# Kernel tuning notes

Measured on AMD Instinct MI355X. Metric: run time of the kernel, lower is better.

Reference implementation:

```python
import jax, jax.numpy as jnp
import numpy as np

EPS = 1e-6
OHEM_RATIO = 3
NUM_KERNELS = 6
ALPHA = 0.5


def _dice_loss(inp, tgt, mask):
    # inp/tgt/mask: [B, H, W] -> scalar mean over batch
    B = inp.shape[0]
    i = (inp * mask).reshape(B, -1)
    t = (tgt * mask).reshape(B, -1)
    inter = jnp.sum(i * t, axis=1)
    union = jnp.sum(i * i, axis=1) + jnp.sum(t * t, axis=1) + EPS
    return jnp.mean(1.0 - 2.0 * inter / union)


def _ohem_mask(pred_prob, gt, tmask, ratio=OHEM_RATIO):
    # Vectorized per-sample OHEM: keep all positives plus the top
    # min(ratio*n_pos, n_neg) highest-scoring negatives.
    B, H, W = pred_prob.shape
    p = pred_prob.reshape(B, -1)
    g = gt.reshape(B, -1)
    m = tmask.reshape(B, -1)
    pos = (g > 0.5) & (m > 0.5)
    neg = (g <= 0.5) & (m > 0.5)
    n_pos = jnp.sum(pos, axis=1)
    n_neg = jnp.minimum(ratio * n_pos, jnp.sum(neg, axis=1))  # [B]
    scores = jnp.where(neg, p, -jnp.inf)
    # descending rank of each pixel's score within its sample
    order = jnp.argsort(-scores, axis=1)
    rank = jnp.argsort(order, axis=1)
    hard_neg = neg & (rank < n_neg[:, None])
    return (pos | hard_neg).astype(jnp.float32).reshape(B, H, W)


def setup_inputs() -> dict:
    key = jax.random.key(0)
    k1, k2, k3, k4 = jax.random.split(key, 4)
    B, C, H, W = 16, 6, 640, 640
    pred = jax.random.normal(k1, (B, C, H, W), dtype=jnp.float32)
    gt_text = (jax.random.uniform(k2, (B, 1, H, W)) > 0.9).astype(jnp.float32)
    gt_kernels = (jax.random.uniform(k3, (B, C - 1, H, W)) > 0.9).astype(jnp.float32)
    training_mask = (jax.random.uniform(k4, (B, 1, H, W)) > 0.05).astype(jnp.float32)
    return {"pred": pred, "gt_text": gt_text, "gt_kernels": gt_kernels,
            "training_mask": training_mask}


def reference(pred, gt_text, gt_kernels, training_mask):
    pred_text = pred[:, 0, :, :]                 # [B,H,W]
    pred_kernels = pred[:, 1:, :, :]             # [B,K,H,W]
    gt_text = gt_text[:, 0, :, :]                # squeeze(1)
    tmask = training_mask[:, 0, :, :]

    # original computes sigmoid + OHEM under no_grad -> stop_gradient
    pred_prob = jax.lax.stop_gradient(jax.nn.sigmoid(pred_text))
    ohem = jax.lax.stop_gradient(_ohem_mask(pred_prob, gt_text, tmask))

    loss_text = _dice_loss(pred_prob, gt_text, ohem)

    # vectorized dice over the K=num_kernels-1 kernel maps, mask broadcast
    pk = jax.nn.sigmoid(pred_kernels)            # [B,K,H,W]
    m = tmask[:, None, :, :]
    i = pk * m
    t = gt_kernels * m
    inter = jnp.sum(i * t, axis=(2, 3))          # [B,K]
    union = jnp.sum(i * i, axis=(2, 3)) + jnp.sum(t * t, axis=(2, 3)) + EPS
    # mean over kernels of (mean over batch) == mean over (B,K)
    loss_kernels = jnp.mean(1.0 - 2.0 * inter / union)

    loss = loss_kernels + ALPHA * loss_text
    return (loss, loss_text, loss_kernels)
```

## Files before the change

kernel.cpp:

```cpp
#include <hip/hip_runtime.h>
#include <math.h>

#define HW 409600
#define BB 16
#define CPRED 6
#define NKER 5
#define NBINS 2048
#define CHUNKS 128
#define EPSF 1e-6f

__device__ __forceinline__ float sigmoidf_(float x) {
    return 1.0f / (1.0f + __expf(-x));
}

__device__ __forceinline__ void proc_text(float m, float x, float g,
    float& n_pos, float& n_neg, float& sp, float& sp2,
    float* s_cnt, float* s_p2)
{
    if (m > 0.5f) {
        float p = sigmoidf_(x);
        if (g > 0.5f) {
            n_pos += 1.f; sp += p; sp2 += p * p;
        } else {
            n_neg += 1.f;
            int bin = (int)(p * (float)NBINS);
            bin = bin < 0 ? 0 : (bin > NBINS - 1 ? NBINS - 1 : bin);
            atomicAdd(&s_cnt[bin], 1.f);
            atomicAdd(&s_p2[bin], p * p);
        }
    }
}

__global__ __launch_bounds__(256) void pass1_kernel(
    const float* __restrict__ pred, const float* __restrict__ gt_text,
    const float* __restrict__ gt_k, const float* __restrict__ tmask,
    float* __restrict__ hist_cnt, float* __restrict__ hist_p2,
    float* __restrict__ bstats, float* __restrict__ kstats)
{
    __shared__ float s_cnt[NBINS];
    __shared__ float s_p2[NBINS];
    __shared__ float s_red[19][4];

    const int b = blockIdx.y;
    const int chunk = blockIdx.x;
    const int tid = threadIdx.x;

    for (int i = tid; i < NBINS; i += 256) { s_cnt[i] = 0.f; s_p2[i] = 0.f; }
    __syncthreads();

    const int NV4 = HW / 4;
    const float4* tm4 = reinterpret_cast<const float4*>(tmask + (size_t)b * HW);
    const float4* gt4 = reinterpret_cast<const float4*>(gt_text + (size_t)b * HW);
    const float4* pt4 = reinterpret_cast<const float4*>(pred + (size_t)b * CPRED * HW);
    const float4* gk4 = reinterpret_cast<const float4*>(gt_k + (size_t)b * NKER * HW);

    const int per = NV4 / CHUNKS;
    const int i0 = chunk * per;
    const int i1 = i0 + per;

    float n_pos = 0.f, n_neg = 0.f, sp = 0.f, sp2 = 0.f;
    float kin[NKER], kui[NKER], kut[NKER];
    #pragma unroll
    for (int c = 0; c < NKER; ++c) { kin[c] = 0.f; kui[c] = 0.f; kut[c] = 0.f; }

    for (int i = i0 + tid; i < i1; i += 256) {
        float4 m4 = tm4[i];
        float4 g4 = gt4[i];
        float4 x4 = pt4[i];

        proc_text(m4.x, x4.x, g4.x, n_pos, n_neg, sp, sp2, s_cnt, s_p2);
        proc_text(m4.y, x4.y, g4.y, n_pos, n_neg, sp, sp2, s_cnt, s_p2);
        proc_text(m4.z, x4.z, g4.z, n_pos, n_neg, sp, sp2, s_cnt, s_p2);
        proc_text(m4.w, x4.w, g4.w, n_pos, n_neg, sp, sp2, s_cnt, s_p2);

        float mb0 = m4.x > 0.5f ? 1.f : 0.f;
        float mb1 = m4.y > 0.5f ? 1.f : 0.f;
        float mb2 = m4.z > 0.5f ? 1.f : 0.f;
        float mb3 = m4.w > 0.5f ? 1.f : 0.f;

        #pragma unroll
        for (int c = 0; c < NKER; ++c) {
            float4 xk = pt4[(size_t)(c + 1) * NV4 + i];
            float4 gg = gk4[(size_t)c * NV4 + i];
            float p0 = sigmoidf_(xk.x), p1 = sigmoidf_(xk.y);
            float p2 = sigmoidf_(xk.z), p3 = sigmoidf_(xk.w);
            kin[c] += mb0 * p0 * gg.x + mb1 * p1 * gg.y
                    + mb2 * p2 * gg.z + mb3 * p3 * gg.w;
            kui[c] += mb0 * p0 * p0 + mb1 * p1 * p1
                    + mb2 * p2 * p2 + mb3 * p3 * p3;
            kut[c] += mb0 * gg.x + mb1 * gg.y + mb2 * gg.z + mb3 * gg.w;
        }
    }

    const int lane = tid & 63;
    const int wv = tid >> 6;
    #define WRED(v) { for (int o_ = 32; o_ > 0; o_ >>= 1) v += __shfl_down(v, o_, 64); }
    WRED(n_pos) WRED(n_neg) WRED(sp) WRED(sp2)
    if (lane == 0) {
        s_red[0][wv] = n_pos; s_red[1][wv] = n_neg;
        s_red[2][wv] = sp;    s_red[3][wv] = sp2;
    }
    #pragma unroll
    for (int c = 0; c < NKER; ++c) {
        float a = kin[c], u = kui[c], t = kut[c];
        WRED(a) WRED(u) WRED(t)
        if (lane == 0) {
            s_red[4 + c * 3 + 0][wv] = a;
            s_red[4 + c * 3 + 1][wv] = u;
            s_red[4 + c * 3 + 2][wv] = t;
        }
    }
    #undef WRED
    __syncthreads();

    if (tid < 19) {
        float a = s_red[tid][0] + s_red[tid][1] + s_red[tid][2] + s_red[tid][3];
        float* dst;
        if (tid < 4) dst = &bstats[b * 4 + tid];
        else {
            int q = tid - 4;
            dst = &kstats[(b * NKER + q / 3) * 3 + (q % 3)];
        }
        atomicAdd(dst, a);
    }

    for (int i = tid; i < NBINS; i += 256) {
        float c = s_cnt[i];
        if (c != 0.f) {
            atomicAdd(&hist_cnt[b * NBINS + i], c);
            atomicAdd(&hist_p2[b * NBINS + i], s_p2[i]);
        }
    }
}

__global__ __launch_bounds__(1024) void finalize_kernel(
    const float* __restrict__ hist_cnt, const float* __restrict__ hist_p2,
    const float* __restrict__ bstats, const float* __restrict__ kstats,
    float* __restrict__ out)
{
    __shared__ float s_text[BB];
    __shared__ float s_kterm[BB * NKER];

    const int tid = threadIdx.x;
    const int w = tid >> 6;
    const int lane = tid & 63;
    const int SEG = NBINS / 64;

    float cg = 0.f, pg = 0.f;
    {
        int base = w * NBINS + lane * SEG;
        for (int k = 0; k < SEG; ++k) {
            cg += hist_cnt[base + k];
            pg += hist_p2[base + k];
        }
    }
    float pc = cg, pp = pg;
    #pragma unroll
    for (int o = 1; o < 64; o <<= 1) {
        float tc = __shfl_up(pc, o, 64);
        float tp = __shfl_up(pp, o, 64);
        if (lane >= o) { pc += tc; pp += tp; }
    }
    float totc = __shfl(pc, 63, 64);
    float totp = __shfl(pp, 63, 64);
    float sufc = totc - pc;
    float sufp = totp - pp;

    float n_pos  = bstats[w * 4 + 0];
    float n_negt = bstats[w * 4 + 1];
    float sp     = bstats[w * 4 + 2];
    float sp2    = bstats[w * 4 + 3];
    float n_sel  = fminf(3.0f * n_pos, n_negt);

    float hard_p2 = 0.f;
    bool cross = (sufc < n_sel) && (sufc + cg >= n_sel);
    unsigned long long bal = __ballot(cross);
    if (n_sel <= 0.f) {
        hard_p2 = 0.f;
    } else if (bal == 0ULL) {
        hard_p2 = totp;
    } else {
        int ls = 63 - __builtin_clzll(bal);
        float run  = __shfl(sufc, ls, 64);
        float runp = __shfl(sufp, ls, 64);
        float bc = 0.f, bp = 0.f;
        if (lane < SEG) {
            int idx = w * NBINS + ls * SEG + lane;
            bc = hist_cnt[idx];
            bp = hist_p2[idx];
        }
        float pc2 = bc, pp2 = bp;
        #pragma unroll
        for (int o = 1; o < 64; o <<= 1) {
            float tc = __shfl_up(pc2, o, 64);
            float tp = __shfl_up(pp2, o, 64);
            if (lane >= o) { pc2 += tc; pp2 += tp; }
        }
        float tot2c = __shfl(pc2, SEG - 1, 64);
        float tot2p = __shfl(pp2, SEG - 1, 64);
        float suf2c = tot2c - pc2;
        float suf2p = tot2p - pp2;
        bool cross2 = (lane < SEG) && (run + suf2c < n_sel) && (run + suf2c + bc >= n_sel);
        unsigned long long bal2 = __ballot(cross2);
        if (bal2 == 0ULL) {
            hard_p2 = runp + tot2p;
        } else {
            int ks = 63 - __builtin_clzll(bal2);
            float rs  = __shfl(suf2c, ks, 64);
            float rsp = __shfl(suf2p, ks, 64);
            float cc  = __shfl(bc, ks, 64);
            float cp  = __shfl(bp, ks, 64);
            float need = n_sel - (run + rs);
            hard_p2 = runp + rsp + (cc > 0.f ? cp * (need / cc) : 0.f);
        }
    }

    if (lane == 0) {
        float uni = sp2 + n_pos + hard_p2 + EPSF;
        s_text[w] = 1.0f - 2.0f * sp / uni;
    }
    __syncthreads();

    if (tid < BB * NKER) {
        float a = kstats[tid * 3 + 0];
        float u = kstats[tid * 3 + 1];
        float t = kstats[tid * 3 + 2];
        s_kterm[tid] = 1.0f - 2.0f * a / (u + t + EPSF);
    }
    __syncthreads();

    if (tid == 0) {
        float lt = 0.f;
        for (int b2 = 0; b2 < BB; ++b2) lt += s_text[b2];
        lt /= (float)BB;
        float lk = 0.f;
        for (int j = 0; j < BB * NKER; ++j) lk += s_kterm[j];
        lk /= (float)(BB * NKER);
        out[0] = lk + 0.5f * lt;
        out[1] = lt;
        out[2] = lk;
    }
}

extern "C" void kernel_launch(void* const* d_in, const int* in_sizes, int n_in,
                              void* d_out, int out_size, void* d_ws, size_t ws_size,
                              hipStream_t stream)
{
    const float* pred    = (const float*)d_in[0];
    const float* gt_text = (const float*)d_in[1];
    const float* gt_k    = (const float*)d_in[2];
    const float* tmask   = (const float*)d_in[3];

    float* ws = (float*)d_ws;
    float* hist_cnt = ws;
    float* hist_p2  = ws + (size_t)BB * NBINS;
    float* bstats   = ws + (size_t)2 * BB * NBINS;
    float* kstats   = bstats + BB * 4;

    size_t zero_bytes = ((size_t)2 * BB * NBINS + BB * 4 + BB * NKER * 3) * sizeof(float);
    hipMemsetAsync(d_ws, 0, zero_bytes, stream);

    dim3 grid(CHUNKS, BB), block(256);
    hipLaunchKernelGGL(pass1_kernel, grid, block, 0, stream,
                       pred, gt_text, gt_k, tmask, hist_cnt, hist_p2, bstats, kstats);
    hipLaunchKernelGGL(finalize_kernel, dim3(1), dim3(1024), 0, stream,
                       hist_cnt, hist_p2, bstats, kstats, (float*)d_out);
}
```

Measured before the change: 375.5 us.

## Hoist all channel loads, branchless text path, fewer bins, split finalize

The main loop now issues all eleven float4 loads up front, which gives more memory-level parallelism. The per-pixel text branch becomes branchless arithmetic, with invalid pixels sent to a dummy histogram bin. The histogram shrinks to 1024 bins, the sigmoid uses a hardware reciprocal, and launch bounds request higher occupancy. The single-block finalize is split into a per-batch kernel plus a combine kernel. In exchange, the dummy bin draws atomics from every pixel, coarser bins lower the precision of the OHEM interpolation, and there is one extra launch.

```diff
diff --git a/kernel.cpp b/kernel.cpp
--- a/kernel.cpp
+++ b/kernel.cpp
@@ -5,47 +5,29 @@
 #define BB 16
 #define CPRED 6
 #define NKER 5
-#define NBINS 2048
+#define NBINS 1024
 #define CHUNKS 128
 #define EPSF 1e-6f
 
 __device__ __forceinline__ float sigmoidf_(float x) {
-    return 1.0f / (1.0f + __expf(-x));
-}
-
-__device__ __forceinline__ void proc_text(float m, float x, float g,
-    float& n_pos, float& n_neg, float& sp, float& sp2,
-    float* s_cnt, float* s_p2)
-{
-    if (m > 0.5f) {
-        float p = sigmoidf_(x);
-        if (g > 0.5f) {
-            n_pos += 1.f; sp += p; sp2 += p * p;
-        } else {
-            n_neg += 1.f;
-            int bin = (int)(p * (float)NBINS);
-            bin = bin < 0 ? 0 : (bin > NBINS - 1 ? NBINS - 1 : bin);
-            atomicAdd(&s_cnt[bin], 1.f);
-            atomicAdd(&s_p2[bin], p * p);
-        }
-    }
-}
-
-__global__ __launch_bounds__(256) void pass1_kernel(
+    return __builtin_amdgcn_rcpf(1.0f + __expf(-x));
+}
+
+__global__ __launch_bounds__(256, 8) void pass1_kernel(
     const float* __restrict__ pred, const float* __restrict__ gt_text,
     const float* __restrict__ gt_k, const float* __restrict__ tmask,
     float* __restrict__ hist_cnt, float* __restrict__ hist_p2,
     float* __restrict__ bstats, float* __restrict__ kstats)
 {
-    __shared__ float s_cnt[NBINS];
-    __shared__ float s_p2[NBINS];
+    __shared__ float s_cnt[NBINS + 1];
+    __shared__ float s_p2[NBINS + 1];
     __shared__ float s_red[19][4];
 
     const int b = blockIdx.y;
     const int chunk = blockIdx.x;
     const int tid = threadIdx.x;
 
-    for (int i = tid; i < NBINS; i += 256) { s_cnt[i] = 0.f; s_p2[i] = 0.f; }
+    for (int i = tid; i <= NBINS; i += 256) { s_cnt[i] = 0.f; s_p2[i] = 0.f; }
     __syncthreads();
 
     const int NV4 = HW / 4;
@@ -64,32 +46,54 @@
     for (int c = 0; c < NKER; ++c) { kin[c] = 0.f; kui[c] = 0.f; kut[c] = 0.f; }
 
     for (int i = i0 + tid; i < i1; i += 256) {
-        float4 m4 = tm4[i];
-        float4 g4 = gt4[i];
-        float4 x4 = pt4[i];
-
-        proc_text(m4.x, x4.x, g4.x, n_pos, n_neg, sp, sp2, s_cnt, s_p2);
-        proc_text(m4.y, x4.y, g4.y, n_pos, n_neg, sp, sp2, s_cnt, s_p2);
-        proc_text(m4.z, x4.z, g4.z, n_pos, n_neg, sp, sp2, s_cnt, s_p2);
-        proc_text(m4.w, x4.w, g4.w, n_pos, n_neg, sp, sp2, s_cnt, s_p2);
-
-        float mb0 = m4.x > 0.5f ? 1.f : 0.f;
-        float mb1 = m4.y > 0.5f ? 1.f : 0.f;
-        float mb2 = m4.z > 0.5f ? 1.f : 0.f;
-        float mb3 = m4.w > 0.5f ? 1.f : 0.f;
-
-        #pragma unroll
-        for (int c = 0; c < NKER; ++c) {
-            float4 xk = pt4[(size_t)(c + 1) * NV4 + i];
-            float4 gg = gk4[(size_t)c * NV4 + i];
-            float p0 = sigmoidf_(xk.x), p1 = sigmoidf_(xk.y);
-            float p2 = sigmoidf_(xk.z), p3 = sigmoidf_(xk.w);
-            kin[c] += mb0 * p0 * gg.x + mb1 * p1 * gg.y
-                    + mb2 * p2 * gg.z + mb3 * p3 * gg.w;
-            kui[c] += mb0 * p0 * p0 + mb1 * p1 * p1
-                    + mb2 * p2 * p2 + mb3 * p3 * p3;
-            kut[c] += mb0 * gg.x + mb1 * gg.y + mb2 * gg.z + mb3 * gg.w;
-        }
+        float4 m4  = tm4[i];
+        float4 g4  = gt4[i];
+        float4 x4  = pt4[i];
+        float4 xk0 = pt4[(size_t)1 * NV4 + i];
+        float4 xk1 = pt4[(size_t)2 * NV4 + i];
+        float4 xk2 = pt4[(size_t)3 * NV4 + i];
+        float4 xk3 = pt4[(size_t)4 * NV4 + i];
+        float4 xk4 = pt4[(size_t)5 * NV4 + i];
+        float4 gg0 = gk4[(size_t)0 * NV4 + i];
+        float4 gg1 = gk4[(size_t)1 * NV4 + i];
+        float4 gg2 = gk4[(size_t)2 * NV4 + i];
+        float4 gg3 = gk4[(size_t)3 * NV4 + i];
+        float4 gg4 = gk4[(size_t)4 * NV4 + i];
+
+        #define TEXT1(mm, xx, ggt) { \
+            float p = sigmoidf_(xx); \
+            float posf = (mm) * (ggt); \
+            float negf = (mm) - posf; \
+            float pp_ = p * p; \
+            n_pos += posf; n_neg += negf; \
+            sp += posf * p; sp2 += posf * pp_; \
+            int bin = (int)(p * (float)NBINS); \
+            bin = bin > NBINS - 1 ? NBINS - 1 : bin; \
+            bin = negf > 0.f ? bin : NBINS; \
+            atomicAdd(&s_cnt[bin], 1.f); \
+            atomicAdd(&s_p2[bin], pp_); \
+        }
+        TEXT1(m4.x, x4.x, g4.x)
+        TEXT1(m4.y, x4.y, g4.y)
+        TEXT1(m4.z, x4.z, g4.z)
+        TEXT1(m4.w, x4.w, g4.w)
+        #undef TEXT1
+
+        #define KCH(c, xk, gg) { \
+            float p0 = sigmoidf_(xk.x), p1 = sigmoidf_(xk.y); \
+            float p2_ = sigmoidf_(xk.z), p3 = sigmoidf_(xk.w); \
+            kin[c] += m4.x * p0 * gg.x + m4.y * p1 * gg.y \
+                    + m4.z * p2_ * gg.z + m4.w * p3 * gg.w; \
+            kui[c] += m4.x * p0 * p0 + m4.y * p1 * p1 \
+                    + m4.z * p2_ * p2_ + m4.w * p3 * p3; \
+            kut[c] += m4.x * gg.x + m4.y * gg.y + m4.z * gg.z + m4.w * gg.w; \
+        }
+        KCH(0, xk0, gg0)
+        KCH(1, xk1, gg1)
+        KCH(2, xk2, gg2)
+        KCH(3, xk3, gg3)
+        KCH(4, xk4, gg4)
+        #undef KCH
     }
 
     const int lane = tid & 63;
@@ -133,22 +137,19 @@
     }
 }
 
-__global__ __launch_bounds__(1024) void finalize_kernel(
+__global__ __launch_bounds__(64) void finalize_batch_kernel(
     const float* __restrict__ hist_cnt, const float* __restrict__ hist_p2,
     const float* __restrict__ bstats, const float* __restrict__ kstats,
-    float* __restrict__ out)
-{
-    __shared__ float s_text[BB];
-    __shared__ float s_kterm[BB * NKER];
-
-    const int tid = threadIdx.x;
-    const int w = tid >> 6;
-    const int lane = tid & 63;
+    float* __restrict__ btext, float* __restrict__ bkterm)
+{
+    const int b = blockIdx.x;
+    const int lane = threadIdx.x;
     const int SEG = NBINS / 64;
 
     float cg = 0.f, pg = 0.f;
     {
-        int base = w * NBINS + lane * SEG;
+        int base = b * NBINS + lane * SEG;
+        #pragma unroll
         for (int k = 0; k < SEG; ++k) {
             cg += hist_cnt[base + k];
             pg += hist_p2[base + k];
@@ -166,10 +167,10 @@
     float sufc = totc - pc;
     float sufp = totp - pp;
 
-    float n_pos  = bstats[w * 4 + 0];
-    float n_negt = bstats[w * 4 + 1];
-    float sp     = bstats[w * 4 + 2];
-    float sp2    = bstats[w * 4 + 3];
+    float n_pos  = bstats[b * 4 + 0];
+    float n_negt = bstats[b * 4 + 1];
+    float sp     = bstats[b * 4 + 2];
+    float sp2    = bstats[b * 4 + 3];
     float n_sel  = fminf(3.0f * n_pos, n_negt);
 
     float hard_p2 = 0.f;
@@ -185,7 +186,7 @@
         float runp = __shfl(sufp, ls, 64);
         float bc = 0.f, bp = 0.f;
         if (lane < SEG) {
-            int idx = w * NBINS + ls * SEG + lane;
+            int idx = b * NBINS + ls * SEG + lane;
             bc = hist_cnt[idx];
             bp = hist_p2[idx];
         }
@@ -217,25 +218,31 @@
 
     if (lane == 0) {
         float uni = sp2 + n_pos + hard_p2 + EPSF;
-        s_text[w] = 1.0f - 2.0f * sp / uni;
-    }
-    __syncthreads();
-
-    if (tid < BB * NKER) {
-        float a = kstats[tid * 3 + 0];
-        float u = kstats[tid * 3 + 1];
-        float t = kstats[tid * 3 + 2];
-        s_kterm[tid] = 1.0f - 2.0f * a / (u + t + EPSF);
-    }
-    __syncthreads();
-
-    if (tid == 0) {
-        float lt = 0.f;
-        for (int b2 = 0; b2 < BB; ++b2) lt += s_text[b2];
-        lt /= (float)BB;
-        float lk = 0.f;
-        for (int j = 0; j < BB * NKER; ++j) lk += s_kterm[j];
-        lk /= (float)(BB * NKER);
+        btext[b] = 1.0f - 2.0f * sp / uni;
+    }
+    if (lane < NKER) {
+        int idx = b * NKER + lane;
+        float a = kstats[idx * 3 + 0];
+        float u = kstats[idx * 3 + 1];
+        float t = kstats[idx * 3 + 2];
+        bkterm[idx] = 1.0f - 2.0f * a / (u + t + EPSF);
+    }
+}
+
+__global__ __launch_bounds__(64) void combine_kernel(
+    const float* __restrict__ btext, const float* __restrict__ bkterm,
+    float* __restrict__ out)
+{
+    const int lane = threadIdx.x;
+    float t = (lane < BB) ? btext[lane] : 0.f;
+    float k = bkterm[lane];
+    if (lane < BB * NKER - 64) k += bkterm[64 + lane];
+    #define WRED(v) { for (int o_ = 32; o_ > 0; o_ >>= 1) v += __shfl_down(v, o_, 64); }
+    WRED(t) WRED(k)
+    #undef WRED
+    if (lane == 0) {
+        float lt = t / (float)BB;
+        float lk = k / (float)(BB * NKER);
         out[0] = lk + 0.5f * lt;
         out[1] = lt;
         out[2] = lk;
@@ -256,6 +263,8 @@
     float* hist_p2  = ws + (size_t)BB * NBINS;
     float* bstats   = ws + (size_t)2 * BB * NBINS;
     float* kstats   = bstats + BB * 4;
+    float* btext    = kstats + BB * NKER * 3;
+    float* bkterm   = btext + BB;
 
     size_t zero_bytes = ((size_t)2 * BB * NBINS + BB * 4 + BB * NKER * 3) * sizeof(float);
     hipMemsetAsync(d_ws, 0, zero_bytes, stream);
@@ -263,6 +272,8 @@
     dim3 grid(CHUNKS, BB), block(256);
     hipLaunchKernelGGL(pass1_kernel, grid, block, 0, stream,
                        pred, gt_text, gt_k, tmask, hist_cnt, hist_p2, bstats, kstats);
-    hipLaunchKernelGGL(finalize_kernel, dim3(1), dim3(1024), 0, stream,
-                       hist_cnt, hist_p2, bstats, kstats, (float*)d_out);
-}
+    hipLaunchKernelGGL(finalize_batch_kernel, dim3(BB), dim3(64), 0, stream,
+                       hist_cnt, hist_p2, bstats, kstats, btext, bkterm);
+    hipLaunchKernelGGL(combine_kernel, dim3(1), dim3(64), 0, stream,
+                       btext, bkterm, (float*)d_out);
+}
```

Result: no change. 372.9 us (-0.7%).
